# Kernel optimization log

Hardware: AMD Instinct MI355X
Metric: run time of the kernel (lower is better)

The kernel has to match this reference:

```python
import jax, jax.numpy as jnp
import numpy as np

N_NODES = 50000
N_EDGES = 800000
F_IN = 64
HIDDEN = 128
HEADS = 4
C = HIDDEN // HEADS  # 32 per-head channels
OUT = 256
N_GRAPHS = 1024
BN_EPS = 1e-5
SLOPE = 0.2  # PyG GATConv leaky_relu negative_slope default


def setup_inputs() -> dict:
    key = jax.random.key(0)
    ks = jax.random.split(key, 16)
    x = jax.random.normal(ks[0], (N_NODES, F_IN), dtype=jnp.float32)
    edge_index = jax.random.randint(ks[1], (2, N_EDGES), 0, N_NODES, dtype=jnp.int64)
    batch = jnp.sort(jax.random.randint(ks[2], (N_NODES,), 0, N_GRAPHS, dtype=jnp.int64))
    s = lambda *d: 1.0 / np.sqrt(d[0])
    W1 = jax.random.normal(ks[3], (F_IN, HIDDEN), dtype=jnp.float32) * s(F_IN)
    att_src1 = jax.random.normal(ks[4], (HEADS, C), dtype=jnp.float32) * s(C)
    att_dst1 = jax.random.normal(ks[5], (HEADS, C), dtype=jnp.float32) * s(C)
    b1 = jnp.zeros((HIDDEN,), jnp.float32)
    W2 = jax.random.normal(ks[6], (HIDDEN, HIDDEN), dtype=jnp.float32) * s(HIDDEN)
    att_src2 = jax.random.normal(ks[7], (HEADS, C), dtype=jnp.float32) * s(C)
    att_dst2 = jax.random.normal(ks[8], (HEADS, C), dtype=jnp.float32) * s(C)
    b2 = jnp.zeros((HIDDEN,), jnp.float32)
    bn1_g = jnp.ones((HIDDEN,), jnp.float32); bn1_b = jnp.zeros((HIDDEN,), jnp.float32)
    bn2_g = jnp.ones((HIDDEN,), jnp.float32); bn2_b = jnp.zeros((HIDDEN,), jnp.float32)
    Wlin = jax.random.normal(ks[9], (HIDDEN, OUT), dtype=jnp.float32) * s(HIDDEN)
    blin = jnp.zeros((OUT,), jnp.float32)
    return {"x": x, "edge_index": edge_index, "batch": batch,
            "W1": W1, "att_src1": att_src1, "att_dst1": att_dst1, "b1": b1,
            "W2": W2, "att_src2": att_src2, "att_dst2": att_dst2, "b2": b2,
            "bn1_g": bn1_g, "bn1_b": bn1_b, "bn2_g": bn2_g, "bn2_b": bn2_b,
            "Wlin": Wlin, "blin": blin}


def _gat_conv(x, W, a_src, a_dst, bias, src, dst):
    # x: [N, Fin] -> h: [N, H, C]
    h = (x @ W).reshape(-1, HEADS, C)
    e_src = jnp.sum(h * a_src, axis=-1)  # [N, H]
    e_dst = jnp.sum(h * a_dst, axis=-1)  # [N, H]
    e = jax.nn.leaky_relu(e_src[src] + e_dst[dst], SLOPE)  # [E, H]
    # scatter-softmax over edges grouped by destination node
    m = jax.ops.segment_max(e, dst, num_segments=N_NODES)
    ex = jnp.exp(e - m[dst])
    denom = jax.ops.segment_sum(ex, dst, num_segments=N_NODES)
    alpha = ex / (denom[dst] + 1e-16)  # [E, H]
    out = jax.ops.segment_sum(alpha[:, :, None] * h[src], dst, num_segments=N_NODES)
    return out.reshape(-1, HEADS * C) + bias


def _batchnorm(x, g, b):
    mu = jnp.mean(x, axis=0)
    var = jnp.var(x, axis=0)
    return (x - mu) * jax.lax.rsqrt(var + BN_EPS) * g + b


def reference(x, edge_index, batch, W1, att_src1, att_dst1, b1, W2, att_src2, att_dst2, b2,
              bn1_g, bn1_b, bn2_g, bn2_b, Wlin, blin):
    # PyG GATConv adds self-loops by default
    ar = jnp.arange(N_NODES, dtype=edge_index.dtype)
    src = jnp.concatenate([edge_index[0], ar])
    dst = jnp.concatenate([edge_index[1], ar])
    h = _gat_conv(x, W1, att_src1, att_dst1, b1, src, dst)
    h = jax.nn.elu(_batchnorm(h, bn1_g, bn1_b))
    h = _gat_conv(h, W2, att_src2, att_dst2, b2, src, dst)
    h = jax.nn.elu(_batchnorm(h, bn2_g, bn2_b))
    # global mean pool per graph
    sums = jax.ops.segment_sum(h, batch, num_segments=N_GRAPHS)
    cnts = jax.ops.segment_sum(jnp.ones((N_NODES,), h.dtype), batch, num_segments=N_GRAPHS)
    pooled = sums / jnp.maximum(cnts, 1.0)[:, None]  # [G, HIDDEN]
    return pooled @ Wlin + blin
```

## Files before the change

### kernel.cpp

```cpp
#include <hip/hip_runtime.h>
#include <hip/hip_bf16.h>
#include <hip/hip_fp16.h>
#include <math.h>

#define N_NODES 50000
#define N_EDGES 800000
#define E_TOT   (N_EDGES + N_NODES)
#define F_IN    64
#define HIDDEN  128
#define HEADS   4
#define OUT_DIM 256
#define N_GRAPHS 1024
#define BN_EPS  1e-5f
#define SLOPE   0.2f

#define SCAN_TILE 2048
#define N_TILES   ((N_NODES + SCAN_TILE - 1) / SCAN_TILE)


__global__ void hist_kernel(const int* __restrict__ ei, int* __restrict__ deg) {
    int i = blockIdx.x * blockDim.x + threadIdx.x;
    if (i >= E_TOT) return;
    int d = (i < N_EDGES) ? ei[N_EDGES + i] : (i - N_EDGES);
    atomicAdd(&deg[d], 1);
}

__global__ void scan_partial_kernel(const int* __restrict__ deg, int* __restrict__ tile_sums) {
    __shared__ int wsum[4];
    int tile = blockIdx.x;
    int tid = threadIdx.x;
    int base = tile * SCAN_TILE + tid * 8;
    int s = 0;
    #pragma unroll
    for (int k = 0; k < 8; ++k) {
        int i = base + k;
        if (i < N_NODES) s += deg[i];
    }
    int lane = tid & 63;
    for (int off = 1; off < 64; off <<= 1) s += __shfl_xor(s, off, 64);
    if (lane == 0) wsum[tid >> 6] = s;
    __syncthreads();
    if (tid == 0) tile_sums[tile] = wsum[0] + wsum[1] + wsum[2] + wsum[3];
}

__global__ void scan_tilesums_kernel(const int* __restrict__ tile_sums, int* __restrict__ tile_off) {
    if (threadIdx.x == 0) {
        int acc = 0;
        for (int t = 0; t < N_TILES; ++t) { tile_off[t] = acc; acc += tile_sums[t]; }
    }
}

__global__ void scan_apply_kernel(const int* __restrict__ deg, const int* __restrict__ tile_off,
                                  int* __restrict__ row_start) {
    __shared__ int wsum[4];
    int tile = blockIdx.x;
    int tid = threadIdx.x;
    int lane = tid & 63;
    int wid = tid >> 6;
    int base = tile * SCAN_TILE + tid * 8;
    int v[8];
    int tsum = 0;
    #pragma unroll
    for (int k = 0; k < 8; ++k) {
        int i = base + k;
        v[k] = (i < N_NODES) ? deg[i] : 0;
        tsum += v[k];
    }
    int sc = tsum;
    for (int off = 1; off < 64; off <<= 1) {
        int t = __shfl_up(sc, off, 64);
        if (lane >= off) sc += t;
    }
    if (lane == 63) wsum[wid] = sc;
    __syncthreads();
    int woff = 0;
    for (int w = 0; w < 4; ++w) woff += (w < wid) ? wsum[w] : 0;
    __syncthreads();
    int toff = tile_off[tile] + woff + (sc - tsum);
    #pragma unroll
    for (int k = 0; k < 8; ++k) {
        int i = base + k;
        if (i < N_NODES) row_start[i] = toff;
        toff += v[k];
    }
    if (tile == 0 && tid == 0) row_start[N_NODES] = E_TOT;
}

__global__ void scatter_kernel(const int* __restrict__ ei, const int* __restrict__ row_start,
                               int* __restrict__ cursor, int* __restrict__ csr_src) {
    int i = blockIdx.x * blockDim.x + threadIdx.x;
    if (i >= E_TOT) return;
    int s, d;
    if (i < N_EDGES) { s = ei[i]; d = ei[N_EDGES + i]; }
    else             { s = i - N_EDGES; d = s; }
    int pos = atomicAdd(&cursor[d], 1);
    csr_src[row_start[d] + pos] = s;
}

template<int FIN>
__global__ __launch_bounds__(256) void gemm_att_kernel(
        const float* __restrict__ X, const float* __restrict__ W,
        const float* __restrict__ a_src, const float* __restrict__ a_dst,
        __half* __restrict__ H, float* __restrict__ es, float* __restrict__ ed) {
    int tid = threadIdx.x;
    int cg = tid & 15;
    int np = tid >> 4;
    int n0 = blockIdx.x * 32 + np * 2;
    int n1 = n0 + 1;
    int j0 = cg * 8;
    bool ok0 = n0 < N_NODES, ok1 = n1 < N_NODES;
    const float* x0 = X + (size_t)(ok0 ? n0 : 0) * FIN;
    const float* x1 = X + (size_t)(ok1 ? n1 : 0) * FIN;
    float acc0[8] = {0,0,0,0,0,0,0,0};
    float acc1[8] = {0,0,0,0,0,0,0,0};
    #pragma unroll 2
    for (int k = 0; k < FIN; k += 4) {
        float4 a0 = *reinterpret_cast<const float4*>(x0 + k);
        float4 a1 = *reinterpret_cast<const float4*>(x1 + k);
        #pragma unroll
        for (int kk = 0; kk < 4; ++kk) {
            const float* wr = W + (size_t)(k + kk) * HIDDEN + j0;
            float4 wa = *reinterpret_cast<const float4*>(wr);
            float4 wb = *reinterpret_cast<const float4*>(wr + 4);
            float av0 = (kk == 0) ? a0.x : (kk == 1) ? a0.y : (kk == 2) ? a0.z : a0.w;
            float av1 = (kk == 0) ? a1.x : (kk == 1) ? a1.y : (kk == 2) ? a1.z : a1.w;
            acc0[0] += av0 * wa.x; acc0[1] += av0 * wa.y; acc0[2] += av0 * wa.z; acc0[3] += av0 * wa.w;
            acc0[4] += av0 * wb.x; acc0[5] += av0 * wb.y; acc0[6] += av0 * wb.z; acc0[7] += av0 * wb.w;
            acc1[0] += av1 * wa.x; acc1[1] += av1 * wa.y; acc1[2] += av1 * wa.z; acc1[3] += av1 * wa.w;
            acc1[4] += av1 * wb.x; acc1[5] += av1 * wb.y; acc1[6] += av1 * wb.z; acc1[7] += av1 * wb.w;
        }
    }
    union { __half2 h2[4]; float4 f4; } pk;
    if (ok0) {
        pk.h2[0] = __floats2half2_rn(acc0[0], acc0[1]);
        pk.h2[1] = __floats2half2_rn(acc0[2], acc0[3]);
        pk.h2[2] = __floats2half2_rn(acc0[4], acc0[5]);
        pk.h2[3] = __floats2half2_rn(acc0[6], acc0[7]);
        *reinterpret_cast<float4*>(H + (size_t)n0 * HIDDEN + j0) = pk.f4;
    }
    if (ok1) {
        pk.h2[0] = __floats2half2_rn(acc1[0], acc1[1]);
        pk.h2[1] = __floats2half2_rn(acc1[2], acc1[3]);
        pk.h2[2] = __floats2half2_rn(acc1[4], acc1[5]);
        pk.h2[3] = __floats2half2_rn(acc1[6], acc1[7]);
        *reinterpret_cast<float4*>(H + (size_t)n1 * HIDDEN + j0) = pk.f4;
    }
    float vs0 = 0.f, vd0 = 0.f, vs1 = 0.f, vd1 = 0.f;
    #pragma unroll
    for (int i = 0; i < 8; ++i) {
        float sa = a_src[j0 + i], da = a_dst[j0 + i];
        vs0 += acc0[i] * sa; vd0 += acc0[i] * da;
        vs1 += acc1[i] * sa; vd1 += acc1[i] * da;
    }
    vs0 += __shfl_xor(vs0, 1, 64); vs0 += __shfl_xor(vs0, 2, 64);
    vd0 += __shfl_xor(vd0, 1, 64); vd0 += __shfl_xor(vd0, 2, 64);
    vs1 += __shfl_xor(vs1, 1, 64); vs1 += __shfl_xor(vs1, 2, 64);
    vd1 += __shfl_xor(vd1, 1, 64); vd1 += __shfl_xor(vd1, 2, 64);
    if ((cg & 3) == 0) {
        int h = cg >> 2;
        if (ok0) { es[n0 * HEADS + h] = vs0; ed[n0 * HEADS + h] = vd0; }
        if (ok1) { es[n1 * HEADS + h] = vs1; ed[n1 * HEADS + h] = vd1; }
    }
}

__global__ void gat_aggregate_kernel(const __half* __restrict__ H, const float* __restrict__ es,
                                     const float* __restrict__ ed, const int* __restrict__ row_start,
                                     const int* __restrict__ csr_src, const float* __restrict__ bias,
                                     float* __restrict__ out) {
    int lane = threadIdx.x & 63;
    int n = blockIdx.x * 4 + (threadIdx.x >> 6);
    if (n >= N_NODES) return;
    int hid = lane >> 4;
    float edn = ed[n * HEADS + hid];
    int k0 = row_start[n], k1 = row_start[n + 1];
    const __half2* Hp = reinterpret_cast<const __half2*>(H);
    float dsum = 0.f, accx = 0.f, accy = 0.f;
    int k = k0;
    for (; k + 1 < k1; k += 2) {
        int s0 = csr_src[k];
        int s1 = csr_src[k + 1];
        float e0 = es[s0 * HEADS + hid] + edn;
        float e1 = es[s1 * HEADS + hid] + edn;
        __half2 h0 = Hp[(size_t)s0 * (HIDDEN / 2) + lane];
        __half2 h1 = Hp[(size_t)s1 * (HIDDEN / 2) + lane];
        e0 = (e0 > 0.f) ? e0 : (SLOPE * e0);
        e1 = (e1 > 0.f) ? e1 : (SLOPE * e1);
        float ex0 = __expf(e0);
        float ex1 = __expf(e1);
        float2 f0 = __half22float2(h0);
        float2 f1 = __half22float2(h1);
        dsum += ex0 + ex1;
        accx += ex0 * f0.x + ex1 * f1.x;
        accy += ex0 * f0.y + ex1 * f1.y;
    }
    if (k < k1) {
        int s0 = csr_src[k];
        float e0 = es[s0 * HEADS + hid] + edn;
        __half2 h0 = Hp[(size_t)s0 * (HIDDEN / 2) + lane];
        e0 = (e0 > 0.f) ? e0 : (SLOPE * e0);
        float ex0 = __expf(e0);
        float2 f0 = __half22float2(h0);
        dsum += ex0;
        accx += ex0 * f0.x;
        accy += ex0 * f0.y;
    }
    float inv = 1.f / (dsum + 1e-16f);
    int j = 2 * lane;
    out[(size_t)n * HIDDEN + j]     = accx * inv + bias[j];
    out[(size_t)n * HIDDEN + j + 1] = accy * inv + bias[j + 1];
}

__global__ void bn_stats_kernel(const float* __restrict__ X, float* __restrict__ stats) {
    int c = threadIdx.x & 127;
    int r0 = blockIdx.x * 2 + (threadIdx.x >> 7);
    float s = 0.f, s2 = 0.f;
    for (int n = r0; n < N_NODES; n += gridDim.x * 2) {
        float v = X[(size_t)n * HIDDEN + c];
        s += v;
        s2 += v * v;
    }
    atomicAdd(&stats[c], s);
    atomicAdd(&stats[HIDDEN + c], s2);
}

__global__ void bn_apply_kernel(float* __restrict__ X, const float* __restrict__ stats,
                                const float* __restrict__ g, const float* __restrict__ b) {
    const float invN = 1.f / (float)N_NODES;
    int i = blockIdx.x * blockDim.x + threadIdx.x;
    const int total = N_NODES * HIDDEN;
    for (; i < total; i += gridDim.x * blockDim.x) {
        int c = i & 127;
        float mu = stats[c] * invN;
        float var = stats[HIDDEN + c] * invN - mu * mu;
        float v = (X[i] - mu) * rsqrtf(var + BN_EPS) * g[c] + b[c];
        X[i] = (v > 0.f) ? v : expm1f(v);
    }
}

__global__ void bn_apply_pool_kernel(const float* __restrict__ X, const float* __restrict__ stats,
                                     const float* __restrict__ g, const float* __restrict__ b,
                                     const int* __restrict__ batch,
                                     float* __restrict__ psum, float* __restrict__ pcnt) {
    const float invN = 1.f / (float)N_NODES;
    int i = blockIdx.x * blockDim.x + threadIdx.x;
    const int total = N_NODES * HIDDEN;
    for (; i < total; i += gridDim.x * blockDim.x) {
        int n = i >> 7, c = i & 127;
        float mu = stats[c] * invN;
        float var = stats[HIDDEN + c] * invN - mu * mu;
        float v = (X[i] - mu) * rsqrtf(var + BN_EPS) * g[c] + b[c];
        v = (v > 0.f) ? v : expm1f(v);
        int gidx = batch[n];
        atomicAdd(&psum[gidx * HIDDEN + c], v);
        if (c == 0) atomicAdd(&pcnt[gidx], 1.0f);
    }
}

__global__ void final_kernel(const float* __restrict__ psum, const float* __restrict__ pcnt,
                             const float* __restrict__ Wlin, const float* __restrict__ blin,
                             float* __restrict__ out) {
    int idx = blockIdx.x * blockDim.x + threadIdx.x;
    int g = idx >> 8, o = idx & 255;
    float invc = 1.f / fmaxf(pcnt[g], 1.f);
    float acc = blin[o];
    const float* pr = psum + g * HIDDEN;
    for (int j = 0; j < HIDDEN; ++j)
        acc += pr[j] * invc * Wlin[j * OUT_DIM + o];
    out[idx] = acc;
}


extern "C" void kernel_launch(void* const* d_in, const int* in_sizes, int n_in,
                              void* d_out, int out_size, void* d_ws, size_t ws_size,
                              hipStream_t stream) {
    const float* x    = (const float*)d_in[0];
    const int*   ei   = (const int*)d_in[1];
    const int*   batch= (const int*)d_in[2];
    const float* W1   = (const float*)d_in[3];
    const float* as1  = (const float*)d_in[4];
    const float* ad1  = (const float*)d_in[5];
    const float* b1   = (const float*)d_in[6];
    const float* W2   = (const float*)d_in[7];
    const float* as2  = (const float*)d_in[8];
    const float* ad2  = (const float*)d_in[9];
    const float* b2   = (const float*)d_in[10];
    const float* bn1g = (const float*)d_in[11];
    const float* bn1b = (const float*)d_in[12];
    const float* bn2g = (const float*)d_in[13];
    const float* bn2b = (const float*)d_in[14];
    const float* Wlin = (const float*)d_in[15];
    const float* blin = (const float*)d_in[16];
    float* out = (float*)d_out;

    char* ws = (char*)d_ws;
    const size_t SZ_H = (size_t)N_NODES * HIDDEN * 4;
    __half* A       = (__half*)(ws);
    float* B        = (float*)(ws + SZ_H);
    size_t off = 2 * SZ_H;
    float* es       = (float*)(ws + off); off += (size_t)N_NODES * HEADS * 4;
    float* ed       = (float*)(ws + off); off += (size_t)N_NODES * HEADS * 4;
    int*   row_start= (int*)(ws + off);   off += ((size_t)(N_NODES + 1) * 4 + 511) & ~511ull;
    int*   csr_src  = (int*)(ws + off);   off += ((size_t)E_TOT * 4 + 511) & ~511ull;
    int*   tile_sums= (int*)(ws + off);   off += ((size_t)N_TILES * 4 + 511) & ~511ull;
    int*   tile_off = (int*)(ws + off);   off += ((size_t)N_TILES * 4 + 511) & ~511ull;
    size_t zoff = off;
    int*   deg      = (int*)(ws + off);   off += (size_t)N_NODES * 4;
    int*   cursor   = (int*)(ws + off);   off += (size_t)N_NODES * 4;
    float* stats1   = (float*)(ws + off); off += 2 * HIDDEN * 4;
    float* stats2   = (float*)(ws + off); off += 2 * HIDDEN * 4;
    float* psum     = (float*)(ws + off); off += (size_t)N_GRAPHS * HIDDEN * 4;
    float* pcnt     = (float*)(ws + off); off += (size_t)N_GRAPHS * 4;
    size_t zbytes = off - zoff;
    (void)ws_size; (void)n_in; (void)in_sizes; (void)out_size;

    hipMemsetAsync(ws + zoff, 0, zbytes, stream);

    const int TB = 256;
    const int egrid = (E_TOT + TB - 1) / TB;
    const int ggrid = (N_NODES + 31) / 32;

    hist_kernel<<<egrid, TB, 0, stream>>>(ei, deg);
    scan_partial_kernel<<<N_TILES, TB, 0, stream>>>(deg, tile_sums);
    scan_tilesums_kernel<<<1, 64, 0, stream>>>(tile_sums, tile_off);
    scan_apply_kernel<<<N_TILES, TB, 0, stream>>>(deg, tile_off, row_start);
    scatter_kernel<<<egrid, TB, 0, stream>>>(ei, row_start, cursor, csr_src);

    gemm_att_kernel<F_IN><<<ggrid, TB, 0, stream>>>(x, W1, as1, ad1, A, es, ed);
    gat_aggregate_kernel<<<N_NODES / 4, TB, 0, stream>>>(A, es, ed, row_start, csr_src, b1, B);
    bn_stats_kernel<<<512, TB, 0, stream>>>(B, stats1);
    bn_apply_kernel<<<2048, TB, 0, stream>>>(B, stats1, bn1g, bn1b);

    gemm_att_kernel<HIDDEN><<<ggrid, TB, 0, stream>>>(B, W2, as2, ad2, A, es, ed);
    gat_aggregate_kernel<<<N_NODES / 4, TB, 0, stream>>>(A, es, ed, row_start, csr_src, b2, B);
    bn_stats_kernel<<<512, TB, 0, stream>>>(B, stats2);
    bn_apply_pool_kernel<<<2048, TB, 0, stream>>>(B, stats2, bn2g, bn2b, batch, psum, pcnt);

    final_kernel<<<(N_GRAPHS * OUT_DIM) / TB, TB, 0, stream>>>(psum, pcnt, Wlin, blin, out);
}
```

Before: 562.0 us.

## Stage GEMM weights in shared memory and compute four nodes per thread

The node-feature GEMM kernel now copies the whole weight matrix into LDS at block start, so the inner loop reads weights from LDS instead of global/L1. Each thread now handles four node rows instead of two, giving more register reuse of each weight load, and the grid is halved to match. The trade-off is LDS use of 64 KB for the HIDDEN instantiation, which limits occupancy, plus a full weight copy per block and higher register pressure.

```diff
diff --git a/kernel.cpp b/kernel.cpp
--- a/kernel.cpp
+++ b/kernel.cpp
@@ -102,64 +102,74 @@
         const float* __restrict__ X, const float* __restrict__ W,
         const float* __restrict__ a_src, const float* __restrict__ a_dst,
         __half* __restrict__ H, float* __restrict__ es, float* __restrict__ ed) {
+    __shared__ float Wl[FIN * HIDDEN];
     int tid = threadIdx.x;
+    for (int i = tid * 4; i < FIN * HIDDEN; i += 256 * 4) {
+        *reinterpret_cast<float4*>(&Wl[i]) = *reinterpret_cast<const float4*>(&W[i]);
+    }
+    __syncthreads();
+
     int cg = tid & 15;
     int np = tid >> 4;
-    int n0 = blockIdx.x * 32 + np * 2;
-    int n1 = n0 + 1;
+    int nb = blockIdx.x * 64 + np * 4;
     int j0 = cg * 8;
-    bool ok0 = n0 < N_NODES, ok1 = n1 < N_NODES;
-    const float* x0 = X + (size_t)(ok0 ? n0 : 0) * FIN;
-    const float* x1 = X + (size_t)(ok1 ? n1 : 0) * FIN;
-    float acc0[8] = {0,0,0,0,0,0,0,0};
-    float acc1[8] = {0,0,0,0,0,0,0,0};
-    #pragma unroll 2
+
+    bool ok[4];
+    const float* xp[4];
+    #pragma unroll
+    for (int t = 0; t < 4; ++t) {
+        ok[t] = (nb + t) < N_NODES;
+        xp[t] = X + (size_t)(ok[t] ? nb + t : 0) * FIN;
+    }
+    float acc[4][8];
+    #pragma unroll
+    for (int t = 0; t < 4; ++t)
+        #pragma unroll
+        for (int c = 0; c < 8; ++c) acc[t][c] = 0.f;
+
     for (int k = 0; k < FIN; k += 4) {
-        float4 a0 = *reinterpret_cast<const float4*>(x0 + k);
-        float4 a1 = *reinterpret_cast<const float4*>(x1 + k);
+        float4 xa[4];
+        #pragma unroll
+        for (int t = 0; t < 4; ++t) xa[t] = *reinterpret_cast<const float4*>(xp[t] + k);
         #pragma unroll
         for (int kk = 0; kk < 4; ++kk) {
-            const float* wr = W + (size_t)(k + kk) * HIDDEN + j0;
-            float4 wa = *reinterpret_cast<const float4*>(wr);
-            float4 wb = *reinterpret_cast<const float4*>(wr + 4);
-            float av0 = (kk == 0) ? a0.x : (kk == 1) ? a0.y : (kk == 2) ? a0.z : a0.w;
-            float av1 = (kk == 0) ? a1.x : (kk == 1) ? a1.y : (kk == 2) ? a1.z : a1.w;
-            acc0[0] += av0 * wa.x; acc0[1] += av0 * wa.y; acc0[2] += av0 * wa.z; acc0[3] += av0 * wa.w;
-            acc0[4] += av0 * wb.x; acc0[5] += av0 * wb.y; acc0[6] += av0 * wb.z; acc0[7] += av0 * wb.w;
-            acc1[0] += av1 * wa.x; acc1[1] += av1 * wa.y; acc1[2] += av1 * wa.z; acc1[3] += av1 * wa.w;
-            acc1[4] += av1 * wb.x; acc1[5] += av1 * wb.y; acc1[6] += av1 * wb.z; acc1[7] += av1 * wb.w;
+            const float4 wA = *reinterpret_cast<const float4*>(&Wl[(k + kk) * HIDDEN + j0]);
+            const float4 wB = *reinterpret_cast<const float4*>(&Wl[(k + kk) * HIDDEN + j0 + 4]);
+            #pragma unroll
+            for (int t = 0; t < 4; ++t) {
+                float xv = (kk == 0) ? xa[t].x : (kk == 1) ? xa[t].y : (kk == 2) ? xa[t].z : xa[t].w;
+                acc[t][0] += xv * wA.x; acc[t][1] += xv * wA.y;
+                acc[t][2] += xv * wA.z; acc[t][3] += xv * wA.w;
+                acc[t][4] += xv * wB.x; acc[t][5] += xv * wB.y;
+                acc[t][6] += xv * wB.z; acc[t][7] += xv * wB.w;
+            }
         }
     }
-    union { __half2 h2[4]; float4 f4; } pk;
-    if (ok0) {
-        pk.h2[0] = __floats2half2_rn(acc0[0], acc0[1]);
-        pk.h2[1] = __floats2half2_rn(acc0[2], acc0[3]);
-        pk.h2[2] = __floats2half2_rn(acc0[4], acc0[5]);
-        pk.h2[3] = __floats2half2_rn(acc0[6], acc0[7]);
-        *reinterpret_cast<float4*>(H + (size_t)n0 * HIDDEN + j0) = pk.f4;
-    }
-    if (ok1) {
-        pk.h2[0] = __floats2half2_rn(acc1[0], acc1[1]);
-        pk.h2[1] = __floats2half2_rn(acc1[2], acc1[3]);
-        pk.h2[2] = __floats2half2_rn(acc1[4], acc1[5]);
-        pk.h2[3] = __floats2half2_rn(acc1[6], acc1[7]);
-        *reinterpret_cast<float4*>(H + (size_t)n1 * HIDDEN + j0) = pk.f4;
-    }
-    float vs0 = 0.f, vd0 = 0.f, vs1 = 0.f, vd1 = 0.f;
-    #pragma unroll
-    for (int i = 0; i < 8; ++i) {
-        float sa = a_src[j0 + i], da = a_dst[j0 + i];
-        vs0 += acc0[i] * sa; vd0 += acc0[i] * da;
-        vs1 += acc1[i] * sa; vd1 += acc1[i] * da;
-    }
-    vs0 += __shfl_xor(vs0, 1, 64); vs0 += __shfl_xor(vs0, 2, 64);
-    vd0 += __shfl_xor(vd0, 1, 64); vd0 += __shfl_xor(vd0, 2, 64);
-    vs1 += __shfl_xor(vs1, 1, 64); vs1 += __shfl_xor(vs1, 2, 64);
-    vd1 += __shfl_xor(vd1, 1, 64); vd1 += __shfl_xor(vd1, 2, 64);
-    if ((cg & 3) == 0) {
-        int h = cg >> 2;
-        if (ok0) { es[n0 * HEADS + h] = vs0; ed[n0 * HEADS + h] = vd0; }
-        if (ok1) { es[n1 * HEADS + h] = vs1; ed[n1 * HEADS + h] = vd1; }
+
+    #pragma unroll
+    for (int t = 0; t < 4; ++t) {
+        int n = nb + t;
+        if (ok[t]) {
+            union { __half2 h2[4]; float4 f4; } pk;
+            pk.h2[0] = __floats2half2_rn(acc[t][0], acc[t][1]);
+            pk.h2[1] = __floats2half2_rn(acc[t][2], acc[t][3]);
+            pk.h2[2] = __floats2half2_rn(acc[t][4], acc[t][5]);
+            pk.h2[3] = __floats2half2_rn(acc[t][6], acc[t][7]);
+            *reinterpret_cast<float4*>(H + (size_t)n * HIDDEN + j0) = pk.f4;
+        }
+        float vs = 0.f, vd = 0.f;
+        #pragma unroll
+        for (int c = 0; c < 8; ++c) {
+            vs += acc[t][c] * a_src[j0 + c];
+            vd += acc[t][c] * a_dst[j0 + c];
+        }
+        vs += __shfl_xor(vs, 1, 64); vs += __shfl_xor(vs, 2, 64);
+        vd += __shfl_xor(vd, 1, 64); vd += __shfl_xor(vd, 2, 64);
+        if ((cg & 3) == 0 && ok[t]) {
+            int h = cg >> 2;
+            es[n * HEADS + h] = vs;
+            ed[n * HEADS + h] = vd;
+        }
     }
 }
 
@@ -317,7 +327,7 @@
 
     const int TB = 256;
     const int egrid = (E_TOT + TB - 1) / TB;
-    const int ggrid = (N_NODES + 31) / 32;
+    const int ggrid = (N_NODES + 63) / 64;
 
     hist_kernel<<<egrid, TB, 0, stream>>>(ei, deg);
     scan_partial_kernel<<<N_TILES, TB, 0, stream>>>(deg, tile_sums);
```

Result: faster. 513.0 us (-8.7%).
